# Kernel tuning notes

Measured on AMD Instinct MI355X. Metric: run time of the kernel, lower is better.

## Reference

```python
import jax, jax.numpy as jnp
import numpy as np


def sobel_kernels_3d(dtype=jnp.float32):
    # Standard 3D Sobel: derivative [-1,0,1] along one axis, smoothing [1,2,1]
    # along the other two. Returns shape (3, 1, 3, 3, 3) in OIDHW layout.
    s = jnp.array([1.0, 2.0, 1.0], dtype=dtype)
    d = jnp.array([-1.0, 0.0, 1.0], dtype=dtype)
    kd = jnp.einsum('i,j,k->ijk', d, s, s)  # d/dD
    kh = jnp.einsum('i,j,k->ijk', s, d, s)  # d/dH
    kw = jnp.einsum('i,j,k->ijk', s, s, d)  # d/dW
    return jnp.stack([kd, kh, kw], axis=0)[:, None]  # (3,1,3,3,3)


def _grad3d(x, kernels):
    # x: (B, C, D, H, W) -> flatten (B*C, 1, D, H, W), conv with padding=1.
    B, C, D, H, W = x.shape
    x_ = x.reshape(B * C, 1, D, H, W)
    return jax.lax.conv_general_dilated(
        x_, kernels.astype(x.dtype),
        window_strides=(1, 1, 1),
        padding=((1, 1), (1, 1), (1, 1)),
        dimension_numbers=('NCDHW', 'OIDHW', 'NCDHW'),
    )  # (B*C, 3, D, H, W)


def setup_inputs() -> dict:
    key = jax.random.key(0)
    k1, k2 = jax.random.split(key)
    shape = (4, 4, 64, 128, 128)
    pred = jax.random.normal(k1, shape, dtype=jnp.float32)
    target = jax.random.normal(k2, shape, dtype=jnp.float32)
    return {"pred": pred, "target": target}


def reference(pred, target):
    kernels = sobel_kernels_3d(pred.dtype)
    grad_pred = _grad3d(pred, kernels)
    grad_target = _grad3d(target, kernels)
    # loss_type == 'l1'
    return jnp.mean(jnp.abs(grad_pred - grad_target))
```

## Files before the change

### kernel.cpp

```cpp
#include <hip/hip_runtime.h>

#define NB 16
#define DD 64
#define HH 128
#define WW 128
#define HW (HH * WW)

constexpr int TH = 8;
constexpr int LY = TH + 2;
constexpr int PL = LY * WW;
constexpr int RING = 6;
constexpr int NT = 8;
constexpr int NQ = 4;
constexpr int SLOTS = 3;
constexpr float INV_COUNT = 1.0f / 50331648.0f;

__global__ void zero_out_kernel(float* out) {
    if (threadIdx.x == 0 && blockIdx.x == 0) out[0] = 0.0f;
}

__global__ __launch_bounds__(256, 4) void sobel_l1_kernel(
    const float* __restrict__ pred,
    const float* __restrict__ target,
    float* __restrict__ out)
{
    __shared__ float ring[RING * PL];

    const int tid = threadIdx.x;
    int b = blockIdx.x;
    const int bh = b & 15; b >>= 4;
    const int q  = b & 3;  b >>= 2;
    const int bn = b;

    const int h0 = bh * TH;
    const int dbase = q * (NT * 2);
    const size_t nbase = (size_t)bn * (size_t)(DD * HW);

    const bool k2ok = tid < 128;
    int  soff[SLOTS];
    int  stoff[SLOTS];
    int  sz[SLOTS];
    bool sokh[SLOTS];
#pragma unroll
    for (int k = 0; k < SLOTS; ++k) {
        const int i  = (k < 2) ? (k * 256 + tid) : (512 + (tid & 127));
        const int z  = i / 320;
        const int r  = i - z * 320;
        const int y  = r >> 5;
        const int q4 = r & 31;
        const int gh = h0 - 1 + y;
        sokh[k]  = (unsigned)gh < HH;
        soff[k]  = min(max(gh, 0), HH - 1) * WW + 4 * q4;
        stoff[k] = y * WW + 4 * q4;
        sz[k]    = z;
    }

    float4 sp[SLOTS], sq[SLOTS];

    auto load_pair = [&](int p0) {
#pragma unroll
        for (int k = 0; k < SLOTS; ++k) {
            if (k < 2 || k2ok) {
                const int gd  = dbase + p0 + sz[k];
                const int gdc = min(max(gd, 0), DD - 1);
                const size_t idx = nbase + (size_t)gdc * HW + soff[k];
                sp[k] = *(const float4*)(pred + idx);
                sq[k] = *(const float4*)(target + idx);
            }
        }
    };

    auto store_pair = [&](int p0) {
        const int base0 = ((p0 + 1) % RING) * PL;
        const int base1 = ((p0 + 2) % RING) * PL;
#pragma unroll
        for (int k = 0; k < SLOTS; ++k) {
            if (k < 2 || k2ok) {
                const int gd = dbase + p0 + sz[k];
                const float m = (sokh[k] && (unsigned)gd < DD) ? 1.0f : 0.0f;
                float* dst = &ring[(sz[k] ? base1 : base0) + stoff[k]];
                *(float4*)dst = float4{(sp[k].x - sq[k].x) * m,
                                       (sp[k].y - sq[k].y) * m,
                                       (sp[k].z - sq[k].z) * m,
                                       (sp[k].w - sq[k].w) * m};
            }
        }
    };

    const int tc = tid & 31;
    const int lh = tid >> 5;

    auto compute_tile = [&](int tau, float& acc) {
        auto plane_l = [&](int base, float4& A_, float4& Bh_, float4& Bw_) {
            float4 rs[3], rdw[3];
#pragma unroll
            for (int r = 0; r < 3; ++r) {
                const float4 v = *(const float4*)&ring[base + (lh + r) * WW + 4 * tc];
                float lm = __shfl_up(v.w, 1, 32);
                float rp = __shfl_down(v.x, 1, 32);
                if (tc == 0)  lm = 0.f;
                if (tc == 31) rp = 0.f;
                rs[r]  = float4{lm  + 2.f * v.x + v.y,
                                v.x + 2.f * v.y + v.z,
                                v.y + 2.f * v.z + v.w,
                                v.z + 2.f * v.w + rp};
                rdw[r] = float4{v.y - lm, v.z - v.x, v.w - v.y, rp - v.z};
            }
            A_  = float4{rs[0].x + 2.f * rs[1].x + rs[2].x,
                         rs[0].y + 2.f * rs[1].y + rs[2].y,
                         rs[0].z + 2.f * rs[1].z + rs[2].z,
                         rs[0].w + 2.f * rs[1].w + rs[2].w};
            Bh_ = float4{rs[2].x - rs[0].x, rs[2].y - rs[0].y,
                         rs[2].z - rs[0].z, rs[2].w - rs[0].w};
            Bw_ = float4{rdw[0].x + 2.f * rdw[1].x + rdw[2].x,
                         rdw[0].y + 2.f * rdw[1].y + rdw[2].y,
                         rdw[0].z + 2.f * rdw[1].z + rdw[2].z,
                         rdw[0].w + 2.f * rdw[1].w + rdw[2].w};
        };

        int sb[4];
#pragma unroll
        for (int j = 0; j < 4; ++j) sb[j] = ((2 * tau + j) % RING) * PL;

        float4 rA[3], rBh[3], rBw[3];
        plane_l(sb[0], rA[0], rBh[0], rBw[0]);
        plane_l(sb[1], rA[1], rBh[1], rBw[1]);
#pragma unroll
        for (int ld = 0; ld < 2; ++ld) {
            const int s0 = ld % 3, s1 = (ld + 1) % 3, s2 = (ld + 2) % 3;
            plane_l(sb[ld + 2], rA[s2], rBh[s2], rBw[s2]);
            const float4 a0 = rA[s0],  a2 = rA[s2];
            const float4 b0 = rBh[s0], b1 = rBh[s1], b2 = rBh[s2];
            const float4 c0 = rBw[s0], c1 = rBw[s1], c2 = rBw[s2];
            acc += fabsf(a2.x - a0.x) + fabsf(a2.y - a0.y)
                 + fabsf(a2.z - a0.z) + fabsf(a2.w - a0.w);
            acc += fabsf(b0.x + 2.f * b1.x + b2.x) + fabsf(b0.y + 2.f * b1.y + b2.y)
                 + fabsf(b0.z + 2.f * b1.z + b2.z) + fabsf(b0.w + 2.f * b1.w + b2.w);
            acc += fabsf(c0.x + 2.f * c1.x + c2.x) + fabsf(c0.y + 2.f * c1.y + c2.y)
                 + fabsf(c0.z + 2.f * c1.z + c2.z) + fabsf(c0.w + 2.f * c1.w + c2.w);
        }
    };

    load_pair(-1); store_pair(-1);
    load_pair(1);  store_pair(1);
    __syncthreads();

    float acc = 0.0f;
    for (int tau = 0; tau < NT; ++tau) {
        if (tau + 1 < NT) load_pair(2 * tau + 3);
        compute_tile(tau, acc);
        if (tau + 1 < NT) store_pair(2 * tau + 3);
        __syncthreads();
    }

#pragma unroll
    for (int off = 32; off > 0; off >>= 1)
        acc += __shfl_down(acc, off, 64);
    if ((tid & 63) == 0) ring[tid >> 6] = acc;
    __syncthreads();
    if (tid == 0) {
        const float s = ring[0] + ring[1] + ring[2] + ring[3];
        atomicAdd(out, s * INV_COUNT);
    }
}

extern "C" void kernel_launch(void* const* d_in, const int* in_sizes, int n_in,
                              void* d_out, int out_size, void* d_ws, size_t ws_size,
                              hipStream_t stream) {
    const float* pred   = (const float*)d_in[0];
    const float* target = (const float*)d_in[1];
    float* out = (float*)d_out;

    zero_out_kernel<<<1, 64, 0, stream>>>(out);

    const int nblocks = NB * NQ * (HH / TH);
    sobel_l1_kernel<<<nblocks, 256, 0, stream>>>(pred, target, out);
}
```

Before: 156.5 us.

## Carry per-plane Sobel partials across tiles instead of recomputing overlap planes

Each tile previously rebuilt partial sums for four depth planes, two of which overlapped the previous tile. Now the last two plane partials stay in registers and only two new planes are computed per tile. This removes redundant LDS reads and shuffle work. The ring grows to 8 slots so indexing is static under a 4-way unroll, and launch bounds drop from 4 to 3 blocks per SM to allow more registers. The cost is larger shared memory and lower occupancy.

Result: slower. 208.9 us (+33.5%).

```diff
diff --git a/kernel.cpp b/kernel.cpp
--- a/kernel.cpp
+++ b/kernel.cpp
@@ -9,7 +9,7 @@
 constexpr int TH = 8;
 constexpr int LY = TH + 2;
 constexpr int PL = LY * WW;
-constexpr int RING = 6;
+constexpr int RING = 8;
 constexpr int NT = 8;
 constexpr int NQ = 4;
 constexpr int SLOTS = 3;
@@ -19,7 +19,9 @@
     if (threadIdx.x == 0 && blockIdx.x == 0) out[0] = 0.0f;
 }
 
-__global__ __launch_bounds__(256, 4) void sobel_l1_kernel(
+struct Part { float4 A, Bh, Bw; };
+
+__global__ __launch_bounds__(256, 3) void sobel_l1_kernel(
     const float* __restrict__ pred,
     const float* __restrict__ target,
     float* __restrict__ out)
@@ -90,67 +92,81 @@
     const int tc = tid & 31;
     const int lh = tid >> 5;
 
-    auto compute_tile = [&](int tau, float& acc) {
-        auto plane_l = [&](int base, float4& A_, float4& Bh_, float4& Bw_) {
-            float4 rs[3], rdw[3];
+    auto make_partial = [&](int slot, Part& P) {
+        const int base = slot * PL + lh * WW + 4 * tc;
+        const float4 v0 = *(const float4*)&ring[base];
+        const float4 v1 = *(const float4*)&ring[base + WW];
+        const float4 v2 = *(const float4*)&ring[base + 2 * WW];
+        float4 rs[3], rdw[3];
+        const float4 vv[3] = {v0, v1, v2};
 #pragma unroll
-            for (int r = 0; r < 3; ++r) {
-                const float4 v = *(const float4*)&ring[base + (lh + r) * WW + 4 * tc];
-                float lm = __shfl_up(v.w, 1, 32);
-                float rp = __shfl_down(v.x, 1, 32);
-                if (tc == 0)  lm = 0.f;
-                if (tc == 31) rp = 0.f;
-                rs[r]  = float4{lm  + 2.f * v.x + v.y,
-                                v.x + 2.f * v.y + v.z,
-                                v.y + 2.f * v.z + v.w,
-                                v.z + 2.f * v.w + rp};
-                rdw[r] = float4{v.y - lm, v.z - v.x, v.w - v.y, rp - v.z};
-            }
-            A_  = float4{rs[0].x + 2.f * rs[1].x + rs[2].x,
-                         rs[0].y + 2.f * rs[1].y + rs[2].y,
-                         rs[0].z + 2.f * rs[1].z + rs[2].z,
-                         rs[0].w + 2.f * rs[1].w + rs[2].w};
-            Bh_ = float4{rs[2].x - rs[0].x, rs[2].y - rs[0].y,
-                         rs[2].z - rs[0].z, rs[2].w - rs[0].w};
-            Bw_ = float4{rdw[0].x + 2.f * rdw[1].x + rdw[2].x,
-                         rdw[0].y + 2.f * rdw[1].y + rdw[2].y,
-                         rdw[0].z + 2.f * rdw[1].z + rdw[2].z,
-                         rdw[0].w + 2.f * rdw[1].w + rdw[2].w};
-        };
+        for (int r = 0; r < 3; ++r) {
+            const float4 v = vv[r];
+            float lm = __shfl_up(v.w, 1, 32);
+            float rp = __shfl_down(v.x, 1, 32);
+            if (tc == 0)  lm = 0.f;
+            if (tc == 31) rp = 0.f;
+            rs[r]  = float4{lm  + 2.f * v.x + v.y,
+                            v.x + 2.f * v.y + v.z,
+                            v.y + 2.f * v.z + v.w,
+                            v.z + 2.f * v.w + rp};
+            rdw[r] = float4{v.y - lm, v.z - v.x, v.w - v.y, rp - v.z};
+        }
+        P.A  = float4{rs[0].x + 2.f * rs[1].x + rs[2].x,
+                      rs[0].y + 2.f * rs[1].y + rs[2].y,
+                      rs[0].z + 2.f * rs[1].z + rs[2].z,
+                      rs[0].w + 2.f * rs[1].w + rs[2].w};
+        P.Bh = float4{rs[2].x - rs[0].x, rs[2].y - rs[0].y,
+                      rs[2].z - rs[0].z, rs[2].w - rs[0].w};
+        P.Bw = float4{rdw[0].x + 2.f * rdw[1].x + rdw[2].x,
+                      rdw[0].y + 2.f * rdw[1].y + rdw[2].y,
+                      rdw[0].z + 2.f * rdw[1].z + rdw[2].z,
+                      rdw[0].w + 2.f * rdw[1].w + rdw[2].w};
+    };
 
-        int sb[4];
-#pragma unroll
-        for (int j = 0; j < 4; ++j) sb[j] = ((2 * tau + j) % RING) * PL;
-
-        float4 rA[3], rBh[3], rBw[3];
-        plane_l(sb[0], rA[0], rBh[0], rBw[0]);
-        plane_l(sb[1], rA[1], rBh[1], rBw[1]);
-#pragma unroll
-        for (int ld = 0; ld < 2; ++ld) {
-            const int s0 = ld % 3, s1 = (ld + 1) % 3, s2 = (ld + 2) % 3;
-            plane_l(sb[ld + 2], rA[s2], rBh[s2], rBw[s2]);
-            const float4 a0 = rA[s0],  a2 = rA[s2];
-            const float4 b0 = rBh[s0], b1 = rBh[s1], b2 = rBh[s2];
-            const float4 c0 = rBw[s0], c1 = rBw[s1], c2 = rBw[s2];
-            acc += fabsf(a2.x - a0.x) + fabsf(a2.y - a0.y)
-                 + fabsf(a2.z - a0.z) + fabsf(a2.w - a0.w);
-            acc += fabsf(b0.x + 2.f * b1.x + b2.x) + fabsf(b0.y + 2.f * b1.y + b2.y)
-                 + fabsf(b0.z + 2.f * b1.z + b2.z) + fabsf(b0.w + 2.f * b1.w + b2.w);
-            acc += fabsf(c0.x + 2.f * c1.x + c2.x) + fabsf(c0.y + 2.f * c1.y + c2.y)
-                 + fabsf(c0.z + 2.f * c1.z + c2.z) + fabsf(c0.w + 2.f * c1.w + c2.w);
-        }
+    float acc = 0.0f;
+    auto combine = [&](const Part& Q0, const Part& Q1, const Part& Q2) {
+        const float4 a0 = Q0.A,  a2 = Q2.A;
+        const float4 b0 = Q0.Bh, b1 = Q1.Bh, b2 = Q2.Bh;
+        const float4 c0 = Q0.Bw, c1 = Q1.Bw, c2 = Q2.Bw;
+        acc += fabsf(a2.x - a0.x) + fabsf(a2.y - a0.y)
+             + fabsf(a2.z - a0.z) + fabsf(a2.w - a0.w);
+        acc += fabsf(b0.x + 2.f * b1.x + b2.x) + fabsf(b0.y + 2.f * b1.y + b2.y)
+             + fabsf(b0.z + 2.f * b1.z + b2.z) + fabsf(b0.w + 2.f * b1.w + b2.w);
+        acc += fabsf(c0.x + 2.f * c1.x + c2.x) + fabsf(c0.y + 2.f * c1.y + c2.y)
+             + fabsf(c0.z + 2.f * c1.z + c2.z) + fabsf(c0.w + 2.f * c1.w + c2.w);
     };
 
     load_pair(-1); store_pair(-1);
     load_pair(1);  store_pair(1);
     __syncthreads();
 
-    float acc = 0.0f;
-    for (int tau = 0; tau < NT; ++tau) {
-        if (tau + 1 < NT) load_pair(2 * tau + 3);
-        compute_tile(tau, acc);
-        if (tau + 1 < NT) store_pair(2 * tau + 3);
-        __syncthreads();
+    Part P0, P1, P2, P3;
+    make_partial(0, P0);
+    make_partial(1, P1);
+
+    for (int tj = 0; tj < 2; ++tj) {
+#pragma unroll
+        for (int u = 0; u < 4; ++u) {
+            const int tau = 4 * tj + u;
+            const bool pf = (tau + 1 < NT);
+            if (pf) load_pair(2 * tau + 3);
+            const int sa = (2 * u + 2) % RING;
+            const int sb = (2 * u + 3) % RING;
+            if ((u & 1) == 0) {
+                make_partial(sa, P2);
+                make_partial(sb, P3);
+                combine(P0, P1, P2);
+                combine(P1, P2, P3);
+            } else {
+                make_partial(sa, P0);
+                make_partial(sb, P1);
+                combine(P2, P3, P0);
+                combine(P3, P0, P1);
+            }
+            if (pf) store_pair(2 * tau + 3);
+            __syncthreads();
+        }
     }
 
 #pragma unroll
```
